# Optimization experiments

Measured on AMD Instinct MI355X. Metric: run time of the kernel, lower is better.

## Reference

```python
import jax, jax.numpy as jnp
import numpy as np

N = 50000      # nodes
E = 800000     # edges (avg degree 16)
H = 4          # heads
C = 64         # per-head dim (= hidden_dim, TransformerConv out_channels)
D = H * C      # 256, concat output dim
VOCAB = 100


def setup_inputs() -> dict:
    key = jax.random.key(0)
    ks = jax.random.split(key, 16)
    f = lambda k, shape: (jax.random.normal(k, shape, jnp.float32) * 0.05)
    return {
        "x": jax.random.randint(ks[0], (N,), 0, VOCAB),
        "edge_index": jax.random.randint(ks[1], (2, E), 0, N),
        "embed": f(ks[2], (VOCAB, C)),        # node_embed table (hidden_dim=64)
        "Wq": f(ks[3], (C, D)), "bq": f(ks[4], (D,)),
        "Wk": f(ks[5], (C, D)), "bk": f(ks[6], (D,)),
        "Wv": f(ks[7], (C, D)), "bv": f(ks[8], (D,)),
        "Wskip": f(ks[9], (C, D)), "bskip": f(ks[10], (D,)),
        "Wbeta": f(ks[11], (3 * D, 1)),       # lin_beta has no bias in PyG
        "Wcoop": f(ks[12], (D, 1)), "bcoop": f(ks[13], (1,)),
        "Wanom": f(ks[14], (D, 1)), "banom": f(ks[15], (1,)),
    }


def _segment_softmax(logits, seg, num_segments):
    # logits: [E, H], seg: [E] destination-node ids
    m = jax.ops.segment_max(logits, seg, num_segments=num_segments)   # [N, H]
    ex = jnp.exp(logits - m[seg])
    s = jax.ops.segment_sum(ex, seg, num_segments=num_segments)       # [N, H]
    return ex / (s[seg] + 1e-16)


def _transformer_conv(h, src, dst, Wq, bq, Wk, bk, Wv, bv, Wskip, bskip, Wbeta):
    # h: [N, C] node features; src->dst edges; PyG TransformerConv(beta=True)
    q = (h @ Wq + bq).reshape(N, H, C)
    k = (h @ Wk + bk).reshape(N, H, C)
    v = (h @ Wv + bv).reshape(N, H, C)
    # per-edge attention logits: query of dst, key of src
    logits = (q[dst] * k[src]).sum(-1) / np.sqrt(C)    # [E, H]
    alpha = _segment_softmax(logits, dst, N)           # softmax over in-edges of dst
    msg = v[src] * alpha[..., None]                    # [E, H, C]
    out = jax.ops.segment_sum(msg, dst, num_segments=N).reshape(N, D)
    # beta-gated skip connection
    x_r = h @ Wskip + bskip                            # [N, D]
    beta = jax.nn.sigmoid(jnp.concatenate([out, x_r, out - x_r], axis=-1) @ Wbeta)
    return beta * x_r + (1.0 - beta) * out             # [N, D]


def reference(x, edge_index, embed, Wq, bq, Wk, bk, Wv, bv,
              Wskip, bskip, Wbeta, Wcoop, bcoop, Wanom, banom):
    h = embed[x]                                       # long input -> embedding
    src, dst = edge_index[0], edge_index[1]
    h = _transformer_conv(h, src, dst, Wq, bq, Wk, bk, Wv, bv, Wskip, bskip, Wbeta)
    h = jax.nn.relu(h)                                 # dropout is identity (eval)
    cooperation = jax.nn.sigmoid(h @ Wcoop + bcoop)    # [N, 1]
    anomaly = jax.nn.sigmoid(h @ Wanom + banom)        # [N, 1]
    return cooperation, anomaly, h
```

## Files before the change

kernel.cpp:

```cpp
#include <hip/hip_runtime.h>
#include <hip/hip_bf16.h>
#include <hip/hip_fp16.h>

typedef __hip_bfloat16 bf16;

#define NN 50000
#define EE 800000
#define VOCABSZ 100
#define DD 256
#define NW 25
#define MAXD 64
#define NBUCK 500
#define BNODES 100
#define AWG 500
#define EPW 1600
#define PCAP 24

static __device__ __forceinline__ float b2f(bf16 v) { return __bfloat162float(v); }

static __device__ __forceinline__ float ldf(const void* p, int i, int isf32) {
  if (isf32) return ((const float*)p)[i];
  return b2f(((const bf16*)p)[i]);
}

static __device__ __forceinline__ int block_detect(const unsigned short* e16) {
  __shared__ int f;
  if (threadIdx.x == 0) f = 0;
  __syncthreads();
  unsigned int ex = (e16[threadIdx.x] >> 7) & 0xFF;
  unsigned long long any = __ballot(ex >= 128);
  if ((threadIdx.x & 63) == 0 && any) atomicOr(&f, 1);
  __syncthreads();
  return f;
}

__global__ void k_build_tables(const void* __restrict__ embed,
    const void* __restrict__ Wq, const void* __restrict__ bq,
    const void* __restrict__ Wk, const void* __restrict__ bk,
    const void* __restrict__ Wv, const void* __restrict__ bv,
    const void* __restrict__ Ws, const void* __restrict__ bs,
    const void* __restrict__ Wbeta,
    const void* __restrict__ Wcoop, const void* __restrict__ bcoop,
    const void* __restrict__ Wanom, const void* __restrict__ banom,
    float* __restrict__ Qt, float* __restrict__ Kt,
    __half* __restrict__ VtH, __half* __restrict__ StH,
    float* __restrict__ Wf, int* __restrict__ flag)
{
  __shared__ float e[64];
  int isf32 = block_detect((const unsigned short*)embed);
  int t = threadIdx.x;

  if (blockIdx.y == 4) {
    if (blockIdx.x != 0) return;
    Wf[t]       = ldf(Wbeta, t, isf32)       + ldf(Wbeta, 512 + t, isf32);
    Wf[256 + t] = ldf(Wbeta, 256 + t, isf32) - ldf(Wbeta, 512 + t, isf32);
    Wf[512 + t] = ldf(Wcoop, t, isf32);
    Wf[768 + t] = ldf(Wanom, t, isf32);
    if (t == 0) {
      Wf[1024] = ldf(bcoop, 0, isf32);
      Wf[1025] = ldf(banom, 0, isf32);
      flag[0] = isf32;
    }
    return;
  }

  int row = blockIdx.x;
  if (t < 64) e[t] = ldf(embed, row * 64 + t, isf32);
  __syncthreads();
  const void* W; const void* b;
  switch (blockIdx.y) {
    case 0:  W = Wq; b = bq; break;
    case 1:  W = Wk; b = bk; break;
    case 2:  W = Wv; b = bv; break;
    default: W = Ws; b = bs; break;
  }
  float acc;
  if (isf32) {
    const float* w32 = (const float*)W;
    acc = ((const float*)b)[t];
    #pragma unroll 8
    for (int c = 0; c < 64; ++c) acc = fmaf(e[c], w32[c * DD + t], acc);
  } else {
    const bf16* w16 = (const bf16*)W;
    acc = b2f(((const bf16*)b)[t]);
    #pragma unroll 8
    for (int c = 0; c < 64; ++c) acc = fmaf(e[c], b2f(w16[c * DD + t]), acc);
  }
  switch (blockIdx.y) {
    case 0:  Qt[row * DD + t] = acc; break;
    case 1:  Kt[row * DD + t] = acc; break;
    case 2:  VtH[row * DD + t] = __float2half(acc); break;
    default: StH[row * DD + t] = __float2half(acc); break;
  }
}

__global__ void k_build_logits(const float* __restrict__ Qt, const float* __restrict__ Kt,
                               float* __restrict__ Et)
{
  __shared__ float q[DD];
  int a = blockIdx.x;
  q[threadIdx.x] = Qt[a * DD + threadIdx.x];
  __syncthreads();
  for (int idx = threadIdx.x; idx < VOCABSZ * 4; idx += 256) {
    int b = idx >> 2, h = idx & 3;
    const float* kk = Kt + b * DD + h * 64;
    const float* qq = q + h * 64;
    float acc = 0.f;
    #pragma unroll 8
    for (int c = 0; c < 64; ++c) acc += qq[c] * kk[c];
    Et[(a * VOCABSZ + b) * 4 + h] = __expf(acc * 0.125f);
  }
}

__global__ __launch_bounds__(256) void k_scatter2(
    const int4* __restrict__ src4, const int4* __restrict__ dst4,
    const int* __restrict__ x,
    unsigned char* __restrict__ cnt, unsigned short* __restrict__ seg)
{
  __shared__ unsigned int cur[NBUCK];
  const int t = threadIdx.x;
  const unsigned w = blockIdx.x;
  for (int i = t; i < NBUCK; i += 256) cur[i] = 0;
  __syncthreads();
  const int g0 = blockIdx.x * (EPW / 4);
  for (int g = t; g < EPW / 4; g += 256) {
    int4 s = src4[g0 + g];
    int4 d = dst4[g0 + g];
    int xv0 = x[s.x], xv1 = x[s.y], xv2 = x[s.z], xv3 = x[s.w];
    unsigned b0 = (unsigned)d.x / BNODES, b1 = (unsigned)d.y / BNODES;
    unsigned b2 = (unsigned)d.z / BNODES, b3 = (unsigned)d.w / BNODES;
    unsigned p0 = atomicAdd(&cur[b0], 1u);
    unsigned p1 = atomicAdd(&cur[b1], 1u);
    unsigned p2 = atomicAdd(&cur[b2], 1u);
    unsigned p3 = atomicAdd(&cur[b3], 1u);
    if (p0 < PCAP) seg[((size_t)b0 * AWG + w) * PCAP + p0] =
        (unsigned short)(((unsigned)d.x - b0 * BNODES) | ((unsigned)xv0 << 7));
    if (p1 < PCAP) seg[((size_t)b1 * AWG + w) * PCAP + p1] =
        (unsigned short)(((unsigned)d.y - b1 * BNODES) | ((unsigned)xv1 << 7));
    if (p2 < PCAP) seg[((size_t)b2 * AWG + w) * PCAP + p2] =
        (unsigned short)(((unsigned)d.z - b2 * BNODES) | ((unsigned)xv2 << 7));
    if (p3 < PCAP) seg[((size_t)b3 * AWG + w) * PCAP + p3] =
        (unsigned short)(((unsigned)d.w - b3 * BNODES) | ((unsigned)xv3 << 7));
  }
  __syncthreads();
  for (int i = t; i < NBUCK; i += 256) {
    unsigned c = cur[i]; if (c > PCAP) c = PCAP;
    cnt[(size_t)i * AWG + w] = (unsigned char)c;
  }
}

__global__ __launch_bounds__(256) void k_lists(
    const unsigned char* __restrict__ cnt, const unsigned short* __restrict__ seg,
    int* __restrict__ deg, unsigned short* __restrict__ ell16)
{
  __shared__ unsigned int hist[BNODES * NW];
  const int b = blockIdx.x;
  const int t = threadIdx.x;
  for (int i = t; i < BNODES * NW; i += 256) hist[i] = 0;
  __syncthreads();
  for (int w = t; w < AWG; w += 256) {
    const size_t sbase = (size_t)b * AWG + w;
    int c = (int)cnt[sbase];
    if (!c) continue;
    const uint4* sp4 = (const uint4*)(seg + sbase * PCAP);
    uint4 q0 = sp4[0];
    uint4 q1 = sp4[1];
    uint4 q2 = sp4[2];
    unsigned wd[12] = { q0.x, q0.y, q0.z, q0.w, q1.x, q1.y, q1.z, q1.w,
                        q2.x, q2.y, q2.z, q2.w };
    #pragma unroll
    for (int i = 0; i < 12; ++i) {
      unsigned lo = wd[i] & 0xFFFFu;
      unsigned hi = wd[i] >> 16;
      if (2 * i < c)
        atomicAdd(&hist[(lo & 127u) * NW + ((lo >> 7) >> 2)], 1u << (((lo >> 7) & 3) * 8));
      if (2 * i + 1 < c)
        atomicAdd(&hist[(hi & 127u) * NW + ((hi >> 7) >> 2)], 1u << (((hi >> 7) & 3) * 8));
    }
  }
  __syncthreads();
  if (t < BNODES) {
    int n = b * BNODES + t;
    const unsigned int* cw = hist + t * NW;
    unsigned short* dp = ell16 + (size_t)n * MAXD;
    int k = 0;
    #pragma unroll
    for (int w = 0; w < NW; ++w) {
      unsigned word = cw[w];
      if (!word) continue;
      #pragma unroll
      for (int bb = 0; bb < 4; ++bb) {
        unsigned c = (word >> (8 * bb)) & 255u;
        if (c) { if (k < MAXD) dp[k] = (unsigned short)((unsigned)(w * 4 + bb) | (c << 8)); k++; }
      }
    }
    deg[n] = (k < MAXD) ? k : MAXD;
  }
}

__global__ __launch_bounds__(256) void k_node(
    const int* __restrict__ x, const int* __restrict__ deg,
    const unsigned short* __restrict__ ell16,
    const __half* __restrict__ VtH, const __half* __restrict__ StH,
    const float* __restrict__ Et, const float* __restrict__ Wf,
    void* __restrict__ out, const int* __restrict__ flag)
{
  __shared__ uint2 evs[4][2][32][4];
  const int t = threadIdx.x;
  const int lane = t & 63;
  const int wv = t >> 6;
  const int l31 = lane & 31;
  const int half = lane >> 5;
  const int hbase = lane & 32;
  const int n = blockIdx.x * 8 + wv * 2 + half;
  const int cb = l31 << 3;
  const int head = l31 >> 3;

  const int xd = x[n];
  const int dgn = deg[n];
  const int dgA = __shfl(dgn, 0, 64);
  const int dgB = __shfl(dgn, 32, 64);
  const int dmax = max(dgA, dgB);

  unsigned int mye = (l31 < dgn) ? (unsigned int)ell16[(size_t)n * MAXD + l31] : 0u;
  const int myxs = (int)(mye & 255u);
  const float mycnt = (float)(mye >> 8);
  const unsigned rowoff = (unsigned)myxs << 9;

  float4 ev = *reinterpret_cast<const float4*>(Et + xd * (VOCABSZ * 4) + myxs * 4);
  ev.x *= mycnt; ev.y *= mycnt; ev.z *= mycnt; ev.w *= mycnt;
  uint4* evp = reinterpret_cast<uint4*>(&evs[wv][half][l31][0]);
  evp[0] = make_uint4(__float_as_uint(ev.x), rowoff, __float_as_uint(ev.y), rowoff);
  evp[1] = make_uint4(__float_as_uint(ev.z), rowoff, __float_as_uint(ev.w), rowoff);

  union HF8U { uint4 u; __half2 h2[4]; };
  HF8U xru; xru.u = *reinterpret_cast<const uint4*>(StH + xd * DD + cb);
  const float4 wo0 = *reinterpret_cast<const float4*>(Wf + cb);
  const float4 wo1 = *reinterpret_cast<const float4*>(Wf + cb + 4);
  const float4 wx0 = *reinterpret_cast<const float4*>(Wf + 256 + cb);
  const float4 wx1 = *reinterpret_cast<const float4*>(Wf + 256 + cb + 4);

  const uint2* __restrict__ myev = &evs[wv][half][0][head];
  const char* __restrict__ vbase = reinterpret_cast<const char*>(VtH) + (cb << 1);

  float s = 0.f;
  __half2 a0 = __float2half2_rn(0.f), a1 = __float2half2_rn(0.f);
  __half2 a2 = __float2half2_rn(0.f), a3 = __float2half2_rn(0.f);

  const int j1 = (dmax < 32) ? dmax : 32;
  #pragma unroll 4
  for (int j = 0; j < j1; ++j) {
    uint2 ue = myev[j * 4];
    float e = __uint_as_float(ue.x);
    s += e;
    __half2 e2 = __float2half2_rn(e);
    HF8U vv; vv.u = *reinterpret_cast<const uint4*>(vbase + ue.y);
    a0 = __hfma2(e2, vv.h2[0], a0);
    a1 = __hfma2(e2, vv.h2[1], a1);
    a2 = __hfma2(e2, vv.h2[2], a2);
    a3 = __hfma2(e2, vv.h2[3], a3);
  }
  if (dmax > 32) {
    const float* __restrict__ Erow = Et + xd * (VOCABSZ * 4) + head;
    unsigned int mye2 = (l31 + 32 < dgn) ? (unsigned int)ell16[(size_t)n * MAXD + 32 + l31] : 0u;
    for (int j = 32; j < dmax; ++j) {
      unsigned int en = (unsigned int)__shfl((int)mye2, hbase + (j - 32), 64);
      int xs = (int)(en & 255u);
      float e = (float)(en >> 8) * Erow[xs << 2];
      s += e;
      __half2 e2 = __float2half2_rn(e);
      HF8U vv; vv.u = *reinterpret_cast<const uint4*>(vbase + ((unsigned)xs << 9));
      a0 = __hfma2(e2, vv.h2[0], a0);
      a1 = __hfma2(e2, vv.h2[1], a1);
      a2 = __hfma2(e2, vv.h2[2], a2);
      a3 = __hfma2(e2, vv.h2[3], a3);
    }
  }

  const float inv = 1.f / (s + 1e-16f);
  float o[8] = { __low2float(a0)*inv, __high2float(a0)*inv,
                 __low2float(a1)*inv, __high2float(a1)*inv,
                 __low2float(a2)*inv, __high2float(a2)*inv,
                 __low2float(a3)*inv, __high2float(a3)*inv };
  float xr[8] = { __low2float(xru.h2[0]), __high2float(xru.h2[0]),
                  __low2float(xru.h2[1]), __high2float(xru.h2[1]),
                  __low2float(xru.h2[2]), __high2float(xru.h2[2]),
                  __low2float(xru.h2[3]), __high2float(xru.h2[3]) };

  float bp = o[0]*wo0.x + o[1]*wo0.y + o[2]*wo0.z + o[3]*wo0.w
           + o[4]*wo1.x + o[5]*wo1.y + o[6]*wo1.z + o[7]*wo1.w
           + xr[0]*wx0.x + xr[1]*wx0.y + xr[2]*wx0.z + xr[3]*wx0.w
           + xr[4]*wx1.x + xr[5]*wx1.y + xr[6]*wx1.z + xr[7]*wx1.w;
  #pragma unroll
  for (int m = 16; m >= 1; m >>= 1) bp += __shfl_xor(bp, m, 64);
  const float beta = 1.f / (1.f + __expf(-bp));

  const float4 wc0 = *reinterpret_cast<const float4*>(Wf + 512 + cb);
  const float4 wc1 = *reinterpret_cast<const float4*>(Wf + 512 + cb + 4);
  const float4 wa0 = *reinterpret_cast<const float4*>(Wf + 768 + cb);
  const float4 wa1 = *reinterpret_cast<const float4*>(Wf + 768 + cb + 4);
  const float wcv[8] = { wc0.x, wc0.y, wc0.z, wc0.w, wc1.x, wc1.y, wc1.z, wc1.w };
  const float wav[8] = { wa0.x, wa0.y, wa0.z, wa0.w, wa1.x, wa1.y, wa1.z, wa1.w };

  float h[8];
  float pc = 0.f, pa = 0.f;
  #pragma unroll
  for (int j = 0; j < 8; ++j) {
    float hv = beta * xr[j] + (1.f - beta) * o[j];
    hv = fmaxf(hv, 0.f);
    h[j] = hv;
    pc = fmaf(hv, wcv[j], pc);
    pa = fmaf(hv, wav[j], pa);
  }
  #pragma unroll
  for (int m = 16; m >= 1; m >>= 1) {
    pc += __shfl_xor(pc, m, 64);
    pa += __shfl_xor(pa, m, 64);
  }
  const float coop = 1.f / (1.f + __expf(-(pc + Wf[1024])));
  const float anom = 1.f / (1.f + __expf(-(pa + Wf[1025])));

  if (flag[0]) {
    float* fo = (float*)out;
    if (l31 == 0) { fo[n] = coop; fo[NN + n] = anom; }
    float4* hp = reinterpret_cast<float4*>(fo + 2 * NN + (size_t)n * DD + cb);
    hp[0] = make_float4(h[0], h[1], h[2], h[3]);
    hp[1] = make_float4(h[4], h[5], h[6], h[7]);
  } else {
    bf16* bo = (bf16*)out;
    if (l31 == 0) { bo[n] = __float2bfloat16(coop); bo[NN + n] = __float2bfloat16(anom); }
    struct alignas(16) BF8S { bf16 v[8]; } hb;
    #pragma unroll
    for (int j = 0; j < 8; ++j) hb.v[j] = __float2bfloat16(h[j]);
    *reinterpret_cast<BF8S*>(bo + 2 * NN + (size_t)n * DD + cb) = hb;
  }
}

extern "C" void kernel_launch(void* const* d_in, const int* in_sizes, int n_in,
                              void* d_out, int out_size, void* d_ws, size_t ws_size,
                              hipStream_t stream) {
  (void)in_sizes; (void)n_in; (void)out_size; (void)ws_size;
  const int*  x     = (const int*)d_in[0];
  const int*  ei    = (const int*)d_in[1];
  const void* embed = d_in[2];
  const void* Wq = d_in[3];  const void* bq = d_in[4];
  const void* Wk = d_in[5];  const void* bk = d_in[6];
  const void* Wv = d_in[7];  const void* bv = d_in[8];
  const void* Ws = d_in[9];  const void* bs = d_in[10];
  const void* Wbeta = d_in[11];
  const void* Wcoop = d_in[12]; const void* bcoop = d_in[13];
  const void* Wanom = d_in[14]; const void* banom = d_in[15];
  const int* src = ei;
  const int* dst = ei + EE;

  char* base = (char*)d_ws;
  size_t pos = 0;
  auto take = [&](size_t bytes) -> char* {
    char* p = base + pos;
    pos = (pos + bytes + 255) & ~(size_t)255;
    return p;
  };
  float*  Qt  = (float*)take(VOCABSZ * DD * sizeof(float));
  float*  Kt  = (float*)take(VOCABSZ * DD * sizeof(float));
  __half* VtH = (__half*)take(VOCABSZ * DD * sizeof(__half));
  __half* StH = (__half*)take(VOCABSZ * DD * sizeof(__half));
  float*  Et  = (float*)take(VOCABSZ * VOCABSZ * 4 * sizeof(float));
  float*  Wf  = (float*)take(1026 * sizeof(float));
  int*    deg = (int*)take(NN * sizeof(int));
  int*    flag= (int*)take(256 * sizeof(int));
  unsigned char*  cnt   = (unsigned char*)take((size_t)AWG * NBUCK);
  unsigned short* seg   = (unsigned short*)take((size_t)AWG * NBUCK * PCAP * sizeof(unsigned short));
  unsigned short* ell16 = (unsigned short*)take((size_t)NN * MAXD * sizeof(unsigned short));

  k_build_tables<<<dim3(VOCABSZ, 5), 256, 0, stream>>>(
      embed, Wq, bq, Wk, bk, Wv, bv, Ws, bs,
      Wbeta, Wcoop, bcoop, Wanom, banom,
      Qt, Kt, VtH, StH, Wf, flag);
  k_build_logits<<<VOCABSZ, 256, 0, stream>>>(Qt, Kt, Et);

  k_scatter2<<<AWG, 256, 0, stream>>>((const int4*)src, (const int4*)dst, x, cnt, seg);
  k_lists<<<NBUCK, 256, 0, stream>>>(cnt, seg, deg, ell16);

  k_node<<<NN / 8, 256, 0, stream>>>(x, deg, ell16, VtH, StH, Et, Wf, d_out, flag);
}
```

Measured before the change: 159.7 us.

## Merge independent setup kernels into two phased launches and skip unused segment loads

The table-building and edge-scatter kernels are merged into one launch split by block index, and the logit-table and list-building kernels into a second, cutting five launches to three. The aim is to remove launch overhead and let independent work run side by side on the GPU. The list builder also loads the second and third 16-byte chunks of each segment only when the count needs them, saving global reads. The cost is fused kernels whose shared-memory footprint is the union of both parts, which may lower occupancy.

New measurement: 150.4 us. -5.8%, faster.

```diff
diff --git a/kernel.cpp b/kernel.cpp
--- a/kernel.cpp
+++ b/kernel.cpp
@@ -34,7 +34,8 @@
   return f;
 }
 
-__global__ void k_build_tables(const void* __restrict__ embed,
+__global__ __launch_bounds__(256) void k_phase1(
+    const void* __restrict__ embed,
     const void* __restrict__ Wq, const void* __restrict__ bq,
     const void* __restrict__ Wk, const void* __restrict__ bk,
     const void* __restrict__ Wv, const void* __restrict__ bv,
@@ -44,14 +45,55 @@
     const void* __restrict__ Wanom, const void* __restrict__ banom,
     float* __restrict__ Qt, float* __restrict__ Kt,
     __half* __restrict__ VtH, __half* __restrict__ StH,
-    float* __restrict__ Wf, int* __restrict__ flag)
+    float* __restrict__ Wf, int* __restrict__ flag,
+    const int4* __restrict__ src4, const int4* __restrict__ dst4,
+    const int* __restrict__ x,
+    unsigned char* __restrict__ cnt, unsigned short* __restrict__ seg)
 {
   __shared__ float e[64];
+  __shared__ unsigned int cur[NBUCK];
+  const int t = threadIdx.x;
+  const unsigned bx = blockIdx.x;
+
+  if (bx >= 500) {
+    const unsigned w = bx - 500;
+    for (int i = t; i < NBUCK; i += 256) cur[i] = 0;
+    __syncthreads();
+    const int g0 = w * (EPW / 4);
+    for (int g = t; g < EPW / 4; g += 256) {
+      int4 s = src4[g0 + g];
+      int4 d = dst4[g0 + g];
+      int xv0 = x[s.x], xv1 = x[s.y], xv2 = x[s.z], xv3 = x[s.w];
+      unsigned b0 = (unsigned)d.x / BNODES, b1 = (unsigned)d.y / BNODES;
+      unsigned b2 = (unsigned)d.z / BNODES, b3 = (unsigned)d.w / BNODES;
+      unsigned p0 = atomicAdd(&cur[b0], 1u);
+      unsigned p1 = atomicAdd(&cur[b1], 1u);
+      unsigned p2 = atomicAdd(&cur[b2], 1u);
+      unsigned p3 = atomicAdd(&cur[b3], 1u);
+      if (p0 < PCAP) seg[((size_t)b0 * AWG + w) * PCAP + p0] =
+          (unsigned short)(((unsigned)d.x - b0 * BNODES) | ((unsigned)xv0 << 7));
+      if (p1 < PCAP) seg[((size_t)b1 * AWG + w) * PCAP + p1] =
+          (unsigned short)(((unsigned)d.y - b1 * BNODES) | ((unsigned)xv1 << 7));
+      if (p2 < PCAP) seg[((size_t)b2 * AWG + w) * PCAP + p2] =
+          (unsigned short)(((unsigned)d.z - b2 * BNODES) | ((unsigned)xv2 << 7));
+      if (p3 < PCAP) seg[((size_t)b3 * AWG + w) * PCAP + p3] =
+          (unsigned short)(((unsigned)d.w - b3 * BNODES) | ((unsigned)xv3 << 7));
+    }
+    __syncthreads();
+    for (int i = t; i < NBUCK; i += 256) {
+      unsigned c = cur[i]; if (c > PCAP) c = PCAP;
+      cnt[(size_t)i * AWG + w] = (unsigned char)c;
+    }
+    return;
+  }
+
+  const int y = bx / 100;
+  const int row = bx % 100;
+  if (y == 4 && row != 0) return;
+
   int isf32 = block_detect((const unsigned short*)embed);
-  int t = threadIdx.x;
-
-  if (blockIdx.y == 4) {
-    if (blockIdx.x != 0) return;
+
+  if (y == 4) {
     Wf[t]       = ldf(Wbeta, t, isf32)       + ldf(Wbeta, 512 + t, isf32);
     Wf[256 + t] = ldf(Wbeta, 256 + t, isf32) - ldf(Wbeta, 512 + t, isf32);
     Wf[512 + t] = ldf(Wcoop, t, isf32);
@@ -64,11 +106,10 @@
     return;
   }
 
-  int row = blockIdx.x;
   if (t < 64) e[t] = ldf(embed, row * 64 + t, isf32);
   __syncthreads();
   const void* W; const void* b;
-  switch (blockIdx.y) {
+  switch (y) {
     case 0:  W = Wq; b = bq; break;
     case 1:  W = Wk; b = bk; break;
     case 2:  W = Wv; b = bv; break;
@@ -86,7 +127,7 @@
     #pragma unroll 8
     for (int c = 0; c < 64; ++c) acc = fmaf(e[c], b2f(w16[c * DD + t]), acc);
   }
-  switch (blockIdx.y) {
+  switch (y) {
     case 0:  Qt[row * DD + t] = acc; break;
     case 1:  Kt[row * DD + t] = acc; break;
     case 2:  VtH[row * DD + t] = __float2half(acc); break;
@@ -94,68 +135,34 @@
   }
 }
 
-__global__ void k_build_logits(const float* __restrict__ Qt, const float* __restrict__ Kt,
-                               float* __restrict__ Et)
-{
-  __shared__ float q[DD];
-  int a = blockIdx.x;
-  q[threadIdx.x] = Qt[a * DD + threadIdx.x];
-  __syncthreads();
-  for (int idx = threadIdx.x; idx < VOCABSZ * 4; idx += 256) {
-    int b = idx >> 2, h = idx & 3;
-    const float* kk = Kt + b * DD + h * 64;
-    const float* qq = q + h * 64;
-    float acc = 0.f;
-    #pragma unroll 8
-    for (int c = 0; c < 64; ++c) acc += qq[c] * kk[c];
-    Et[(a * VOCABSZ + b) * 4 + h] = __expf(acc * 0.125f);
-  }
-}
-
-__global__ __launch_bounds__(256) void k_scatter2(
-    const int4* __restrict__ src4, const int4* __restrict__ dst4,
-    const int* __restrict__ x,
-    unsigned char* __restrict__ cnt, unsigned short* __restrict__ seg)
-{
-  __shared__ unsigned int cur[NBUCK];
-  const int t = threadIdx.x;
-  const unsigned w = blockIdx.x;
-  for (int i = t; i < NBUCK; i += 256) cur[i] = 0;
-  __syncthreads();
-  const int g0 = blockIdx.x * (EPW / 4);
-  for (int g = t; g < EPW / 4; g += 256) {
-    int4 s = src4[g0 + g];
-    int4 d = dst4[g0 + g];
-    int xv0 = x[s.x], xv1 = x[s.y], xv2 = x[s.z], xv3 = x[s.w];
-    unsigned b0 = (unsigned)d.x / BNODES, b1 = (unsigned)d.y / BNODES;
-    unsigned b2 = (unsigned)d.z / BNODES, b3 = (unsigned)d.w / BNODES;
-    unsigned p0 = atomicAdd(&cur[b0], 1u);
-    unsigned p1 = atomicAdd(&cur[b1], 1u);
-    unsigned p2 = atomicAdd(&cur[b2], 1u);
-    unsigned p3 = atomicAdd(&cur[b3], 1u);
-    if (p0 < PCAP) seg[((size_t)b0 * AWG + w) * PCAP + p0] =
-        (unsigned short)(((unsigned)d.x - b0 * BNODES) | ((unsigned)xv0 << 7));
-    if (p1 < PCAP) seg[((size_t)b1 * AWG + w) * PCAP + p1] =
-        (unsigned short)(((unsigned)d.y - b1 * BNODES) | ((unsigned)xv1 << 7));
-    if (p2 < PCAP) seg[((size_t)b2 * AWG + w) * PCAP + p2] =
-        (unsigned short)(((unsigned)d.z - b2 * BNODES) | ((unsigned)xv2 << 7));
-    if (p3 < PCAP) seg[((size_t)b3 * AWG + w) * PCAP + p3] =
-        (unsigned short)(((unsigned)d.w - b3 * BNODES) | ((unsigned)xv3 << 7));
-  }
-  __syncthreads();
-  for (int i = t; i < NBUCK; i += 256) {
-    unsigned c = cur[i]; if (c > PCAP) c = PCAP;
-    cnt[(size_t)i * AWG + w] = (unsigned char)c;
-  }
-}
-
-__global__ __launch_bounds__(256) void k_lists(
+__global__ __launch_bounds__(256) void k_phase2(
+    const float* __restrict__ Qt, const float* __restrict__ Kt,
+    float* __restrict__ Et,
     const unsigned char* __restrict__ cnt, const unsigned short* __restrict__ seg,
     int* __restrict__ deg, unsigned short* __restrict__ ell16)
 {
+  __shared__ float q[DD];
   __shared__ unsigned int hist[BNODES * NW];
-  const int b = blockIdx.x;
   const int t = threadIdx.x;
+  const unsigned bx = blockIdx.x;
+
+  if (bx < 100) {
+    const int a = bx;
+    q[t] = Qt[a * DD + t];
+    __syncthreads();
+    for (int idx = t; idx < VOCABSZ * 4; idx += 256) {
+      int b = idx >> 2, h = idx & 3;
+      const float* kk = Kt + b * DD + h * 64;
+      const float* qq = q + h * 64;
+      float acc = 0.f;
+      #pragma unroll 8
+      for (int c = 0; c < 64; ++c) acc += qq[c] * kk[c];
+      Et[(a * VOCABSZ + b) * 4 + h] = __expf(acc * 0.125f);
+    }
+    return;
+  }
+
+  const int b = bx - 100;
   for (int i = t; i < BNODES * NW; i += 256) hist[i] = 0;
   __syncthreads();
   for (int w = t; w < AWG; w += 256) {
@@ -164,8 +171,10 @@
     if (!c) continue;
     const uint4* sp4 = (const uint4*)(seg + sbase * PCAP);
     uint4 q0 = sp4[0];
-    uint4 q1 = sp4[1];
-    uint4 q2 = sp4[2];
+    uint4 q1 = make_uint4(0u, 0u, 0u, 0u);
+    uint4 q2 = make_uint4(0u, 0u, 0u, 0u);
+    if (c > 8)  q1 = sp4[1];
+    if (c > 16) q2 = sp4[2];
     unsigned wd[12] = { q0.x, q0.y, q0.z, q0.w, q1.x, q1.y, q1.z, q1.w,
                         q2.x, q2.y, q2.z, q2.w };
     #pragma unroll
@@ -372,14 +381,13 @@
   unsigned short* seg   = (unsigned short*)take((size_t)AWG * NBUCK * PCAP * sizeof(unsigned short));
   unsigned short* ell16 = (unsigned short*)take((size_t)NN * MAXD * sizeof(unsigned short));
 
-  k_build_tables<<<dim3(VOCABSZ, 5), 256, 0, stream>>>(
+  k_phase1<<<1000, 256, 0, stream>>>(
       embed, Wq, bq, Wk, bk, Wv, bv, Ws, bs,
       Wbeta, Wcoop, bcoop, Wanom, banom,
-      Qt, Kt, VtH, StH, Wf, flag);
-  k_build_logits<<<VOCABSZ, 256, 0, stream>>>(Qt, Kt, Et);
-
-  k_scatter2<<<AWG, 256, 0, stream>>>((const int4*)src, (const int4*)dst, x, cnt, seg);
-  k_lists<<<NBUCK, 256, 0, stream>>>(cnt, seg, deg, ell16);
+      Qt, Kt, VtH, StH, Wf, flag,
+      (const int4*)src, (const int4*)dst, x, cnt, seg);
+
+  k_phase2<<<600, 256, 0, stream>>>(Qt, Kt, Et, cnt, seg, deg, ell16);
 
   k_node<<<NN / 8, 256, 0, stream>>>(x, deg, ell16, VtH, StH, Et, Wf, d_out, flag);
 }
```
